# Kernel tuning notes

Hardware: AMD Instinct MI355X
Metric: run time of the kernel (lower is better)

## Reference

```python
import jax, jax.numpy as jnp
import numpy as np

# RosaAttention config constants
H = 16       # num_rosa_heads
KV = 4       # num_rosa_key_value_heads
QKB = 64     # num_rosa_query_key_bits
VB = 64      # num_rosa_value_bits
HID = 2048   # hidden_size
TAU = 1.0    # temperature buffer


def setup_inputs() -> dict:
    key = jax.random.key(0)
    ks = jax.random.split(key, 8)
    B, S = 2, 2048
    sc = 0.02
    return {
        "x": jax.random.normal(ks[0], (B, S, HID), jnp.float32),
        "attention_mask": jnp.ones((B, S), jnp.int32),
        "Wq": jax.random.normal(ks[1], (HID, H * QKB), jnp.float32) * sc,
        "Wk": jax.random.normal(ks[2], (HID, KV * QKB), jnp.float32) * sc,
        "Wv": jax.random.normal(ks[3], (HID, KV * VB), jnp.float32) * sc,
        "Wo": jax.random.normal(ks[4], (H * VB, HID), jnp.float32) * sc,
        "emb0": jnp.full((H, VB), -1e-05, jnp.float32),
        "emb1": jnp.full((H, VB), +1e-05, jnp.float32),
    }


def reference(x, attention_mask, Wq, Wk, Wv, Wo, emb0, emb1):
    B, S, _ = x.shape
    rep = H // KV
    # projections -> [b, s, heads, bits]
    xq = (x @ Wq).reshape(B, S, H, QKB)
    xk = (x @ Wk).reshape(B, S, KV, QKB)
    xv = (x @ Wv).reshape(B, S, KV, VB)
    # repeat_kv: each kv head repeated n_rep times contiguously
    xk = jnp.repeat(xk, rep, axis=2)   # [b, s, H, QKB]
    xv = jnp.repeat(xv, rep, axis=2)   # [b, s, H, VB]
    # soft bit quantization of q/k, tau-scaled bit-similarity score
    qb = jnp.tanh(xq)
    kb = jnp.tanh(xk)
    scores = jnp.einsum('bqhd,bkhd->bhqk', qb, kb) / (TAU * QKB)
    # causal mask + padding mask (mask True = attend)
    causal = jnp.tril(jnp.ones((S, S), bool))
    mask = causal[None, None] & attention_mask.astype(bool)[:, None, None, :]
    scores = jnp.where(mask, scores, jnp.finfo(scores.dtype).min)
    probs = jax.nn.softmax(scores, axis=-1)        # [b, h, q, k]
    # soft-binarized values: per-bit probabilities, attended, then mapped
    # through learned per-head bit embeddings emb0 (bit=0) / emb1 (bit=1)
    vp = jax.nn.sigmoid(xv)                        # [b, s, H, VB]
    ctx = jnp.einsum('bhqk,bkhv->bqhv', probs, vp) # [b, s, H, VB]
    out_bits = ctx * emb1[None, None] + (1.0 - ctx) * emb0[None, None]
    out = out_bits.reshape(B, S, H * VB) @ Wo      # [b, s, HID]
    return out
```

## Files before the change

### kernel.cpp

```cpp
#include <hip/hip_runtime.h>
#include <math.h>

typedef short bf16x8 __attribute__((ext_vector_type(8)));
typedef float f32x4 __attribute__((ext_vector_type(4)));
typedef unsigned int u32x2 __attribute__((ext_vector_type(2)));
typedef unsigned int u32x4 __attribute__((ext_vector_type(4)));

#define MFMA_BF16(A,B,C) __builtin_amdgcn_mfma_f32_16x16x32_bf16(A,B,C,0,0,0)

#define VMCNT(N) asm volatile("s_waitcnt vmcnt(" #N ")" ::: "memory")
#define RBAR() do { asm volatile("" ::: "memory"); __builtin_amdgcn_s_barrier(); \
                    asm volatile("" ::: "memory"); } while (0)


__device__ __forceinline__ unsigned short f2b(float x) {
    union { float f; unsigned int u; } v; v.f = x;
    unsigned int r = v.u + 0x7FFFu + ((v.u >> 16) & 1u);
    return (unsigned short)(r >> 16);
}

__device__ __forceinline__ unsigned int cvtpk(float lo, float hi) {
    unsigned int r;
    asm("v_cvt_pk_bf16_f32 %0, %1, %2" : "=v"(r) : "v"(lo), "v"(hi));
    return r;
}

__device__ __forceinline__ void gload16(const unsigned short* g, unsigned short* l) {
    __builtin_amdgcn_global_load_lds(
        (const __attribute__((address_space(1))) unsigned int*)(g),
        (__attribute__((address_space(3))) unsigned int*)(l),
        16, 0, 0);
}
__device__ __forceinline__ void gload4(const int* g, int* l) {
    __builtin_amdgcn_global_load_lds(
        (const __attribute__((address_space(1))) unsigned int*)(g),
        (__attribute__((address_space(3))) unsigned int*)(l),
        4, 0, 0);
}

__global__ __launch_bounds__(256) void conv_bf16(const float* __restrict__ s,
                                                 unsigned short* __restrict__ d, int n)
{
    int i = blockIdx.x * blockDim.x + threadIdx.x;
    int stride = gridDim.x * blockDim.x;
    for (int idx = i * 4; idx < n; idx += stride * 4) {
        float4 v = *(const float4*)(s + idx);
        ushort4 o;
        o.x = f2b(v.x); o.y = f2b(v.y); o.z = f2b(v.z); o.w = f2b(v.w);
        *(ushort4*)(d + idx) = o;
    }
}

__global__ __launch_bounds__(256) void transp_conv_qkv(const float* __restrict__ Wq,
                                                       const float* __restrict__ Wk,
                                                       const float* __restrict__ Wv,
                                                       unsigned short* __restrict__ dst)
{
    __shared__ float t[32][33];
    const int tx = threadIdx.x, ty = threadIdx.y;
    int bx = blockIdx.x;
    const float* src; int C, cb, dco;
    if (bx < 32)      { src = Wq; C = 1024; cb = bx;      dco = 0; }
    else if (bx < 40) { src = Wk; C = 256;  cb = bx - 32; dco = 1024; }
    else              { src = Wv; C = 256;  cb = bx - 40; dco = 1280; }
    const int c = cb * 32 + tx;
    const int r0 = blockIdx.y * 32;
#pragma unroll
    for (int i = 0; i < 4; ++i)
        t[ty + i * 8][tx] = src[(size_t)(r0 + ty + i * 8) * C + c];
    __syncthreads();
    const int cc = cb * 32 + ty;
#pragma unroll
    for (int i = 0; i < 4; ++i)
        dst[(size_t)(dco + cc + i * 8) * 2048 + r0 + tx] = f2b(t[tx][ty + i * 8]);
}

__global__ __launch_bounds__(256) void transp_conv(const float* __restrict__ src, int R, int C,
                                                   unsigned short* __restrict__ dst, int pitch)
{
    __shared__ float t[32][33];
    const int tx = threadIdx.x, ty = threadIdx.y;
    const int c = blockIdx.x * 32 + tx;
    const int r0 = blockIdx.y * 32;
#pragma unroll
    for (int i = 0; i < 4; ++i)
        t[ty + i * 8][tx] = src[(size_t)(r0 + ty + i * 8) * C + c];
    __syncthreads();
    const int cc = blockIdx.x * 32 + ty;
#pragma unroll
    for (int i = 0; i < 4; ++i)
        dst[(size_t)(cc + i * 8) * pitch + r0 + tx] = f2b(t[tx][ty + i * 8]);
}

__device__ __forceinline__ void stage_g(const unsigned short* AgL, const unsigned short* BgL,
                                        int K, int k0s,
                                        unsigned short* Asb, unsigned short* Bsb, int w)
{
#pragma unroll
    for (int t = 0; t < 4; ++t) {
        const int sub = t >> 1, half = t & 1;
        gload16(AgL + (size_t)(half * 16) * K + k0s + sub * 32,
                Asb + sub * 4096 + (w * 2 + half) * 512);
    }
#pragma unroll
    for (int kk = 0; kk < 2; ++kk)
        gload16(BgL + k0s + kk * 32, Bsb + kk * 2048 + w * 512);
}

template <int MODE>
__global__ __launch_bounds__(256, 3) void gemm_bt_mfma(
    const unsigned short* __restrict__ A,
    const unsigned short* __restrict__ Bt,
    int M, int N, int K,
    float* __restrict__ Cf,
    unsigned short* __restrict__ qh,
    unsigned short* __restrict__ kh,
    unsigned short* __restrict__ vtt)
{
    __shared__ __align__(16) unsigned short As[2][2 * 128 * 32];
    __shared__ __align__(16) unsigned short Bs[2][2 * 64 * 32];

    const int tid = threadIdx.x;
    const int w = tid >> 6, lane = tid & 63, l15 = lane & 15, quad = lane >> 4;
    const int wm = w & 1, wn = w >> 1;
    const int m0 = blockIdx.y * 128, n0 = blockIdx.x * 64;

    const int dsrow = lane >> 2;
    const int dscol = ((lane & 3) ^ ((lane >> 3) & 3)) * 8;
    const int sl8   = (((lane & 15) << 2) | ((lane >> 4) ^ ((lane >> 1) & 3))) * 8;

    f32x4 acc[4][2];
    const f32x4 zero4 = {0.f, 0.f, 0.f, 0.f};
#pragma unroll
    for (int i = 0; i < 4; ++i)
#pragma unroll
        for (int j = 0; j < 2; ++j) acc[i][j] = zero4;

    const unsigned short* AgL = A  + (size_t)(m0 + w * 32 + dsrow) * K + dscol;
    const unsigned short* BgL = Bt + (size_t)(n0 + w * 16 + dsrow) * K + dscol;

    const int NT = K >> 6;
    stage_g(AgL, BgL, K, 0, &As[0][0], &Bs[0][0], w);

    int cb = 0;
    for (int t = 0; t < NT; ++t) {
        if (t + 1 < NT) {
            stage_g(AgL, BgL, K, (t + 1) * 64, &As[cb ^ 1][0], &Bs[cb ^ 1][0], w);
            VMCNT(6);
        } else {
            VMCNT(0);
        }
        RBAR();

        bf16x8 af[4][2], bf[2][2];
#pragma unroll
        for (int kk = 0; kk < 2; ++kk) {
#pragma unroll
            for (int mt = 0; mt < 4; ++mt)
                af[mt][kk] = *(const bf16x8*)&As[cb][kk * 4096 + (wm * 4 + mt) * 512 + sl8];
#pragma unroll
            for (int nt = 0; nt < 2; ++nt)
                bf[nt][kk] = *(const bf16x8*)&Bs[cb][kk * 2048 + (wn * 2 + nt) * 512 + sl8];
        }
#pragma unroll
        for (int kk = 0; kk < 2; ++kk)
#pragma unroll
            for (int mt = 0; mt < 4; ++mt)
#pragma unroll
                for (int nt = 0; nt < 2; ++nt)
                    acc[mt][nt] = MFMA_BF16(af[mt][kk], bf[nt][kk], acc[mt][nt]);

        if (t + 1 < NT) RBAR();
        cb ^= 1;
    }

    if (MODE == 0) {
#pragma unroll
        for (int mt = 0; mt < 4; ++mt)
#pragma unroll
            for (int nt = 0; nt < 2; ++nt) {
                const int gn = n0 + wn * 32 + nt * 16 + l15;
#pragma unroll
                for (int r = 0; r < 4; ++r) {
                    const int gm = m0 + wm * 64 + mt * 16 + quad * 4 + r;
                    Cf[(size_t)gm * N + gn] = acc[mt][nt][r];
                }
            }
    } else {
        if (n0 < 1024) {
#pragma unroll
            for (int mt = 0; mt < 4; ++mt)
#pragma unroll
                for (int nt = 0; nt < 2; ++nt) {
                    const int gn = n0 + wn * 32 + nt * 16 + l15;
#pragma unroll
                    for (int r = 0; r < 4; ++r) {
                        const int gm = m0 + wm * 64 + mt * 16 + quad * 4 + r;
                        qh[(size_t)gm * 1024 + gn] = f2b(tanhf(acc[mt][nt][r]));
                    }
                }
        } else if (n0 < 1280) {
#pragma unroll
            for (int mt = 0; mt < 4; ++mt)
#pragma unroll
                for (int nt = 0; nt < 2; ++nt) {
                    const int gn = n0 + wn * 32 + nt * 16 + l15 - 1024;
#pragma unroll
                    for (int r = 0; r < 4; ++r) {
                        const int gm = m0 + wm * 64 + mt * 16 + quad * 4 + r;
                        kh[(size_t)gm * 256 + gn] = f2b(tanhf(acc[mt][nt][r]));
                    }
                }
        } else {
#pragma unroll
            for (int mt = 0; mt < 4; ++mt)
#pragma unroll
                for (int nt = 0; nt < 2; ++nt) {
                    const int gn = n0 + wn * 32 + nt * 16 + l15 - 1280;
                    const int g = gn >> 6, vv = gn & 63;
                    const int s0 = m0 + wm * 64 + mt * 16 + quad * 4;
                    const int b = s0 >> 11, sl = s0 & 2047;
                    ushort4 pk;
                    unsigned short* pp = (unsigned short*)&pk;
#pragma unroll
                    for (int r = 0; r < 4; ++r) {
                        float sv = 1.0f / (1.0f + __expf(-acc[mt][nt][r]));
                        pp[r] = f2b(sv);
                    }
                    *(ushort4*)&vtt[((size_t)(b * 4 + g) * 64 + vv) * 2048 + sl] = pk;
                }
        }
    }
}

__global__ __launch_bounds__(256, 3) void rosa_attn_mfma(
    const unsigned short* __restrict__ qh,
    const unsigned short* __restrict__ kh,
    const unsigned short* __restrict__ vtt,
    const int* __restrict__ amask,
    const float* __restrict__ emb0,
    const float* __restrict__ emb1,
    unsigned short* __restrict__ ob)
{
    __shared__ __align__(16) unsigned short Ks[2][2][2048];
    __shared__ __align__(16) unsigned short Vs[2][2][2048];
    __shared__ __align__(16) unsigned int   Ps[4][16][36];
    __shared__ int Mski[2][64];

    const int X = blockIdx.x;
    int qa, qb = 0, nq;
    if (X < 8)       { qa = 31 - X; nq = 1; }
    else if (X < 16) { qa = X + 8;  nq = 1; }
    else             { qa = X - 16; qb = 31 - X; nq = 2; }

    const int h = blockIdx.y, b = blockIdx.z, g = h >> 2;
    const int tid = threadIdx.x;
    const int w = tid >> 6, lane = tid & 63, l15 = lane & 15, quad = lane >> 4;

    const int dsrow = lane >> 2;
    const int dscol = ((lane & 3) ^ ((lane >> 3) & 3)) * 8;
    const int sl8   = (((lane & 15) << 2) | ((lane >> 4) ^ ((lane >> 1) & 3))) * 8;

    const unsigned short* kst = kh + (size_t)b * 2048 * 256 + g * 64
                               + (size_t)(w * 16 + dsrow) * 256 + dscol;
    const unsigned short* vst = vtt + ((size_t)(b * 4 + g) * 64 + w * 16 + dsrow) * 2048
                               + dscol;
    const int* mbase = amask + b * 2048;

    const f32x4 zero4 = {0.f, 0.f, 0.f, 0.f};
    const float cexp = 0.0225421100f;

#define STAGE_TILE(k0s, buf)                                               \
    {                                                                      \
        gload16(kst + (size_t)(k0s) * 256,      &Ks[buf][0][w * 512]);     \
        gload16(kst + (size_t)(k0s) * 256 + 32, &Ks[buf][1][w * 512]);     \
        gload16(vst + (k0s),                    &Vs[buf][0][w * 512]);     \
        gload16(vst + (k0s) + 32,               &Vs[buf][1][w * 512]);     \
        if (w == 0) gload4(mbase + (k0s) + lane, &Mski[buf][0]);           \
    }

    for (int hi = 0; hi < nq; ++hi) {
        const int qt = (hi == 0) ? qa : qb;
        const int q0 = qt * 64;
        const int nkt = qt + 1;
        const int qg = q0 + w * 16 + l15;

        const unsigned short* qrow = qh + ((size_t)(b * 2048 + qg) * 16 + h) * 64;
        const bf16x8 qf0 = *(const bf16x8*)(qrow + quad * 8);
        const bf16x8 qf1 = *(const bf16x8*)(qrow + 32 + quad * 8);

        f32x4 oacc[4];
#pragma unroll
        for (int t = 0; t < 4; ++t) oacc[t] = zero4;
        float psum = 0.0f;

        RBAR();
        STAGE_TILE(0, 0)

        int cb = 0;
        for (int kt = 0; kt < nkt; ++kt) {
            if (kt + 1 < nkt) {
                STAGE_TILE((kt + 1) * 64, cb ^ 1)
                if (w == 0) { VMCNT(5); } else { VMCNT(4); }
            } else {
                VMCNT(0);
            }
            RBAR();

            const bool diag = (kt == qt);
            const int ntlim = diag ? (w + 1) : 4;

#pragma unroll
            for (int nt = 0; nt < 4; ++nt) {
                u32x2 pk2;
                if (nt < ntlim) {
                    bf16x8 kf0 = *(const bf16x8*)&Ks[cb][0][nt * 512 + sl8];
                    bf16x8 kf1 = *(const bf16x8*)&Ks[cb][1][nt * 512 + sl8];
                    __builtin_amdgcn_s_setprio(1);
                    f32x4 sc = MFMA_BF16(kf0, qf0, zero4);
                    sc = MFMA_BF16(kf1, qf1, sc);
                    __builtin_amdgcn_s_setprio(0);
                    const int4 m4 = *(const int4*)&Mski[cb][nt * 16 + quad * 4];
                    const int* mm = (const int*)&m4;
                    const bool dnw = diag && (nt == w);
                    float p[4];
#pragma unroll
                    for (int r = 0; r < 4; ++r) {
                        float pv = __builtin_exp2f(sc[r] * cexp);
                        bool valid = (mm[r] != 0);
                        if (dnw) valid = valid && ((quad * 4 + r) <= l15);
                        pv = valid ? pv : 0.0f;
                        psum += pv;
                        p[r] = pv;
                    }
                    pk2[0] = cvtpk(p[0], p[1]);
                    pk2[1] = cvtpk(p[2], p[3]);
                } else {
                    pk2[0] = 0u; pk2[1] = 0u;
                }
                *(u32x2*)&Ps[w][l15][nt * 8 + quad * 2] = pk2;
            }

            const bf16x8 pf0 = __builtin_bit_cast(bf16x8, *(const u32x4*)&Ps[w][l15][quad * 4]);
            const bf16x8 pf1 = __builtin_bit_cast(bf16x8, *(const u32x4*)&Ps[w][l15][16 + quad * 4]);
            __builtin_amdgcn_s_setprio(1);
#pragma unroll
            for (int nt = 0; nt < 4; ++nt) {
                bf16x8 vf0 = *(const bf16x8*)&Vs[cb][0][nt * 512 + sl8];
                bf16x8 vf1 = *(const bf16x8*)&Vs[cb][1][nt * 512 + sl8];
                oacc[nt] = MFMA_BF16(pf0, vf0, oacc[nt]);
                oacc[nt] = MFMA_BF16(pf1, vf1, oacc[nt]);
            }
            __builtin_amdgcn_s_setprio(0);

            if (kt + 1 < nkt) {
                RBAR();
                cb ^= 1;
            }
        }

        float l = psum;
        l += __shfl_xor(l, 16);
        l += __shfl_xor(l, 32);
        float lq[4];
#pragma unroll
        for (int r = 0; r < 4; ++r) lq[r] = __shfl(l, quad * 4 + r);

#pragma unroll
        for (int nt = 0; nt < 4; ++nt) {
            const float e0 = emb0[h * 64 + nt * 16 + l15];
            const float e1 = emb1[h * 64 + nt * 16 + l15];
#pragma unroll
            for (int r = 0; r < 4; ++r) {
                const float ctx = oacc[nt][r] / lq[r];
                const float val = e0 + ctx * (e1 - e0);
                const size_t s_idx = (size_t)(b * 2048 + q0 + w * 16 + quad * 4 + r);
                ob[(s_idx * 16 + h) * 64 + nt * 16 + l15] = f2b(val);
            }
        }
    }
#undef STAGE_TILE
}

extern "C" void kernel_launch(void* const* d_in, const int* in_sizes, int n_in,
                              void* d_out, int out_size, void* d_ws, size_t ws_size,
                              hipStream_t stream)
{
    const float* x    = (const float*)d_in[0];
    const int*   amask= (const int*)d_in[1];
    const float* Wq   = (const float*)d_in[2];
    const float* Wk   = (const float*)d_in[3];
    const float* Wv   = (const float*)d_in[4];
    const float* Wo   = (const float*)d_in[5];
    const float* emb0 = (const float*)d_in[6];
    const float* emb1 = (const float*)d_in[7];
    float* out = (float*)d_out;

    char* base = (char*)d_ws;
    unsigned short* xh    = (unsigned short*)(base);
    unsigned short* ob    = xh;
    unsigned short* Wqkvt = (unsigned short*)(base + (16u << 20));
    unsigned short* Wot   = (unsigned short*)(base + (22u << 20));
    unsigned short* qh    = (unsigned short*)(base + (26u << 20));
    unsigned short* kh    = (unsigned short*)(base + (34u << 20));
    unsigned short* vtt   = (unsigned short*)(base + (36u << 20));

    conv_bf16<<<2048, 256, 0, stream>>>(x, xh, 4096 * 2048);
    transp_conv_qkv<<<dim3(48, 64), dim3(32, 8), 0, stream>>>(Wq, Wk, Wv, Wqkvt);
    transp_conv<<<dim3(64, 32), dim3(32, 8), 0, stream>>>(Wo, 1024, 2048, Wot, 1024);

    gemm_bt_mfma<1><<<dim3(24, 32), 256, 0, stream>>>(xh, Wqkvt, 4096, 1536, 2048,
                                                      nullptr, qh, kh, vtt);
    rosa_attn_mfma<<<dim3(24, 16, 2), 256, 0, stream>>>(qh, kh, vtt, amask, emb0, emb1, ob);
    gemm_bt_mfma<0><<<dim3(32, 32), 256, 0, stream>>>(ob, Wot, 4096, 2048, 1024,
                                                      out, nullptr, nullptr, nullptr);
}
```

Before: 235.3 us.

## Rework attention scheduling: one q-tile per block, precomputed mask flags, swizzled P

Each attention block now handles a single 64-row query tile, with tiles spread across blocks by a rotating pattern. This replaces the old pairing of a short and a long tile into one block, and the grid grows from 24 to 32 tiles per head. The padding mask is pre-scanned once per block into per-tile 'fully valid' flags, so full tiles skip the mask loads and selects, and the per-tile mask staging into LDS is removed. The P scratch buffer drops its padding in favour of an XOR swizzle, and the launch bounds ask for 4 blocks per CU. The risks are load imbalance from a plain causal distribution and register pressure under the higher occupancy target.

```diff
diff --git a/kernel.cpp b/kernel.cpp
--- a/kernel.cpp
+++ b/kernel.cpp
@@ -9,9 +9,9 @@
 #define MFMA_BF16(A,B,C) __builtin_amdgcn_mfma_f32_16x16x32_bf16(A,B,C,0,0,0)
 
 #define VMCNT(N) asm volatile("s_waitcnt vmcnt(" #N ")" ::: "memory")
+#define LGKM0()  asm volatile("s_waitcnt lgkmcnt(0)" ::: "memory")
 #define RBAR() do { asm volatile("" ::: "memory"); __builtin_amdgcn_s_barrier(); \
                     asm volatile("" ::: "memory"); } while (0)
-
 
 __device__ __forceinline__ unsigned short f2b(float x) {
     union { float f; unsigned int u; } v; v.f = x;
@@ -30,12 +30,6 @@
         (const __attribute__((address_space(1))) unsigned int*)(g),
         (__attribute__((address_space(3))) unsigned int*)(l),
         16, 0, 0);
-}
-__device__ __forceinline__ void gload4(const int* g, int* l) {
-    __builtin_amdgcn_global_load_lds(
-        (const __attribute__((address_space(1))) unsigned int*)(g),
-        (__attribute__((address_space(3))) unsigned int*)(l),
-        4, 0, 0);
 }
 
 __global__ __launch_bounds__(256) void conv_bf16(const float* __restrict__ s,
@@ -233,7 +227,7 @@
     }
 }
 
-__global__ __launch_bounds__(256, 3) void rosa_attn_mfma(
+__global__ __launch_bounds__(256, 4) void rosa_attn_mfma(
     const unsigned short* __restrict__ qh,
     const unsigned short* __restrict__ kh,
     const unsigned short* __restrict__ vtt,
@@ -244,22 +238,21 @@
 {
     __shared__ __align__(16) unsigned short Ks[2][2][2048];
     __shared__ __align__(16) unsigned short Vs[2][2][2048];
-    __shared__ __align__(16) unsigned int   Ps[4][16][36];
-    __shared__ int Mski[2][64];
-
-    const int X = blockIdx.x;
-    int qa, qb = 0, nq;
-    if (X < 8)       { qa = 31 - X; nq = 1; }
-    else if (X < 16) { qa = X + 8;  nq = 1; }
-    else             { qa = X - 16; qb = 31 - X; nq = 2; }
-
+    __shared__ __align__(16) unsigned int   Ps[4][16][32];
+
+    const int a = blockIdx.x & 7, m = blockIdx.x >> 3;
     const int h = blockIdx.y, b = blockIdx.z, g = h >> 2;
+    const int hb = h + 16 * b;
+    const int sel = (m + (hb >> 3)) & 3;
+    const int qt = (sel == 0) ? a : (sel == 1) ? 15 - a : (sel == 2) ? 16 + a : 31 - a;
+
     const int tid = threadIdx.x;
     const int w = tid >> 6, lane = tid & 63, l15 = lane & 15, quad = lane >> 4;
 
     const int dsrow = lane >> 2;
     const int dscol = ((lane & 3) ^ ((lane >> 3) & 3)) * 8;
     const int sl8   = (((lane & 15) << 2) | ((lane >> 4) ^ ((lane >> 1) & 3))) * 8;
+    const int pxor  = (l15 & 7) << 2;
 
     const unsigned short* kst = kh + (size_t)b * 2048 * 256 + g * 64
                                + (size_t)(w * 16 + dsrow) * 256 + dscol;
@@ -269,6 +262,20 @@
 
     const f32x4 zero4 = {0.f, 0.f, 0.f, 0.f};
     const float cexp = 0.0225421100f;
+
+    float cm[4];
+#pragma unroll
+    for (int r = 0; r < 4; ++r) cm[r] = (quad * 4 + r <= l15) ? 1.0f : 0.0f;
+
+    const int4 mv0 = *(const int4*)(mbase + tid * 8);
+    const int4 mv1 = *(const int4*)(mbase + tid * 8 + 4);
+
+    const int q0 = qt * 64;
+    const int nkt = qt + 1;
+
+    const unsigned short* qrow = qh + ((size_t)(b * 2048 + q0 + w * 16 + l15) * 16 + h) * 64;
+    const bf16x8 qf0 = *(const bf16x8*)(qrow + quad * 8);
+    const bf16x8 qf1 = *(const bf16x8*)(qrow + 32 + quad * 8);
 
 #define STAGE_TILE(k0s, buf)                                               \
     {                                                                      \
@@ -276,107 +283,117 @@
         gload16(kst + (size_t)(k0s) * 256 + 32, &Ks[buf][1][w * 512]);     \
         gload16(vst + (k0s),                    &Vs[buf][0][w * 512]);     \
         gload16(vst + (k0s) + 32,               &Vs[buf][1][w * 512]);     \
-        if (w == 0) gload4(mbase + (k0s) + lane, &Mski[buf][0]);           \
-    }
-
-    for (int hi = 0; hi < nq; ++hi) {
-        const int qt = (hi == 0) ? qa : qb;
-        const int q0 = qt * 64;
-        const int nkt = qt + 1;
-        const int qg = q0 + w * 16 + l15;
-
-        const unsigned short* qrow = qh + ((size_t)(b * 2048 + qg) * 16 + h) * 64;
-        const bf16x8 qf0 = *(const bf16x8*)(qrow + quad * 8);
-        const bf16x8 qf1 = *(const bf16x8*)(qrow + 32 + quad * 8);
-
-        f32x4 oacc[4];
-#pragma unroll
-        for (int t = 0; t < 4; ++t) oacc[t] = zero4;
-        float psum = 0.0f;
-
+    }
+
+    STAGE_TILE(0, 0)
+
+    const bool f8 = mv0.x && mv0.y && mv0.z && mv0.w && mv1.x && mv1.y && mv1.z && mv1.w;
+    const unsigned long long bal = __ballot(f8);
+    const bool bytefull = ((bal >> ((lane & 7) * 8)) & 0xFFull) == 0xFFull;
+    const unsigned long long bal2 = __ballot(bytefull && (lane < 8));
+    if (lane == 0) Ps[0][0][w] = (unsigned int)(bal2 & 0xFFull);
+    RBAR();
+    const unsigned int mflags = Ps[0][0][0] | (Ps[0][0][1] << 8)
+                              | (Ps[0][0][2] << 16) | (Ps[0][0][3] << 24);
+    LGKM0();
+    RBAR();
+
+    f32x4 oacc[4];
+#pragma unroll
+    for (int t = 0; t < 4; ++t) oacc[t] = zero4;
+    float psum = 0.0f;
+
+    int cb = 0;
+    for (int kt = 0; kt < nkt; ++kt) {
+        if (kt + 1 < nkt) {
+            STAGE_TILE((kt + 1) * 64, cb ^ 1)
+            VMCNT(4);
+        } else {
+            VMCNT(0);
+        }
         RBAR();
-        STAGE_TILE(0, 0)
-
-        int cb = 0;
-        for (int kt = 0; kt < nkt; ++kt) {
-            if (kt + 1 < nkt) {
-                STAGE_TILE((kt + 1) * 64, cb ^ 1)
-                if (w == 0) { VMCNT(5); } else { VMCNT(4); }
-            } else {
-                VMCNT(0);
-            }
-            RBAR();
-
-            const bool diag = (kt == qt);
-            const int ntlim = diag ? (w + 1) : 4;
-
-#pragma unroll
-            for (int nt = 0; nt < 4; ++nt) {
-                u32x2 pk2;
-                if (nt < ntlim) {
-                    bf16x8 kf0 = *(const bf16x8*)&Ks[cb][0][nt * 512 + sl8];
-                    bf16x8 kf1 = *(const bf16x8*)&Ks[cb][1][nt * 512 + sl8];
-                    __builtin_amdgcn_s_setprio(1);
-                    f32x4 sc = MFMA_BF16(kf0, qf0, zero4);
-                    sc = MFMA_BF16(kf1, qf1, sc);
-                    __builtin_amdgcn_s_setprio(0);
-                    const int4 m4 = *(const int4*)&Mski[cb][nt * 16 + quad * 4];
+
+        const int k0 = kt * 64;
+        const bool diag = (kt == qt);
+        const bool full = (mflags >> kt) & 1u;
+        const int ntlim = diag ? (w + 1) : 4;
+
+#pragma unroll
+        for (int nt = 0; nt < 4; ++nt) {
+            u32x2 pk2;
+            if (nt < ntlim) {
+                bf16x8 kf0 = *(const bf16x8*)&Ks[cb][0][nt * 512 + sl8];
+                bf16x8 kf1 = *(const bf16x8*)&Ks[cb][1][nt * 512 + sl8];
+                __builtin_amdgcn_s_setprio(1);
+                f32x4 sc = MFMA_BF16(kf0, qf0, zero4);
+                sc = MFMA_BF16(kf1, qf1, sc);
+                __builtin_amdgcn_s_setprio(0);
+                const bool dnw = diag && (nt == w);
+                float p[4];
+                if (full) {
+                    if (dnw) {
+#pragma unroll
+                        for (int r = 0; r < 4; ++r)
+                            p[r] = __builtin_exp2f(sc[r] * cexp) * cm[r];
+                    } else {
+#pragma unroll
+                        for (int r = 0; r < 4; ++r)
+                            p[r] = __builtin_exp2f(sc[r] * cexp);
+                    }
+                } else {
+                    const int4 m4 = *(const int4*)(mbase + k0 + nt * 16 + quad * 4);
                     const int* mm = (const int*)&m4;
-                    const bool dnw = diag && (nt == w);
-                    float p[4];
 #pragma unroll
                     for (int r = 0; r < 4; ++r) {
                         float pv = __builtin_exp2f(sc[r] * cexp);
-                        bool valid = (mm[r] != 0);
-                        if (dnw) valid = valid && ((quad * 4 + r) <= l15);
-                        pv = valid ? pv : 0.0f;
-                        psum += pv;
-                        p[r] = pv;
+                        if (dnw) pv *= cm[r];
+                        p[r] = (mm[r] != 0) ? pv : 0.0f;
                     }
-                    pk2[0] = cvtpk(p[0], p[1]);
-                    pk2[1] = cvtpk(p[2], p[3]);
-                } else {
-                    pk2[0] = 0u; pk2[1] = 0u;
                 }
-                *(u32x2*)&Ps[w][l15][nt * 8 + quad * 2] = pk2;
+                psum += (p[0] + p[1]) + (p[2] + p[3]);
+                pk2[0] = cvtpk(p[0], p[1]);
+                pk2[1] = cvtpk(p[2], p[3]);
+            } else {
+                pk2[0] = 0u; pk2[1] = 0u;
             }
-
-            const bf16x8 pf0 = __builtin_bit_cast(bf16x8, *(const u32x4*)&Ps[w][l15][quad * 4]);
-            const bf16x8 pf1 = __builtin_bit_cast(bf16x8, *(const u32x4*)&Ps[w][l15][16 + quad * 4]);
-            __builtin_amdgcn_s_setprio(1);
-#pragma unroll
-            for (int nt = 0; nt < 4; ++nt) {
-                bf16x8 vf0 = *(const bf16x8*)&Vs[cb][0][nt * 512 + sl8];
-                bf16x8 vf1 = *(const bf16x8*)&Vs[cb][1][nt * 512 + sl8];
-                oacc[nt] = MFMA_BF16(pf0, vf0, oacc[nt]);
-                oacc[nt] = MFMA_BF16(pf1, vf1, oacc[nt]);
-            }
-            __builtin_amdgcn_s_setprio(0);
-
-            if (kt + 1 < nkt) {
-                RBAR();
-                cb ^= 1;
-            }
-        }
-
-        float l = psum;
-        l += __shfl_xor(l, 16);
-        l += __shfl_xor(l, 32);
-        float lq[4];
-#pragma unroll
-        for (int r = 0; r < 4; ++r) lq[r] = __shfl(l, quad * 4 + r);
-
+            *(u32x2*)&Ps[w][l15][(nt * 8 + quad * 2) ^ pxor] = pk2;
+        }
+
+        const bf16x8 pf0 = __builtin_bit_cast(bf16x8, *(const u32x4*)&Ps[w][l15][(quad * 4) ^ pxor]);
+        const bf16x8 pf1 = __builtin_bit_cast(bf16x8, *(const u32x4*)&Ps[w][l15][(16 + quad * 4) ^ pxor]);
+        __builtin_amdgcn_s_setprio(1);
 #pragma unroll
         for (int nt = 0; nt < 4; ++nt) {
-            const float e0 = emb0[h * 64 + nt * 16 + l15];
-            const float e1 = emb1[h * 64 + nt * 16 + l15];
-#pragma unroll
-            for (int r = 0; r < 4; ++r) {
-                const float ctx = oacc[nt][r] / lq[r];
-                const float val = e0 + ctx * (e1 - e0);
-                const size_t s_idx = (size_t)(b * 2048 + q0 + w * 16 + quad * 4 + r);
-                ob[(s_idx * 16 + h) * 64 + nt * 16 + l15] = f2b(val);
-            }
+            bf16x8 vf0 = *(const bf16x8*)&Vs[cb][0][nt * 512 + sl8];
+            bf16x8 vf1 = *(const bf16x8*)&Vs[cb][1][nt * 512 + sl8];
+            oacc[nt] = MFMA_BF16(pf0, vf0, oacc[nt]);
+            oacc[nt] = MFMA_BF16(pf1, vf1, oacc[nt]);
+        }
+        __builtin_amdgcn_s_setprio(0);
+
+        if (kt + 1 < nkt) {
+            RBAR();
+            cb ^= 1;
+        }
+    }
+
+    float l = psum;
+    l += __shfl_xor(l, 16);
+    l += __shfl_xor(l, 32);
+    float lq[4];
+#pragma unroll
+    for (int r = 0; r < 4; ++r) lq[r] = __shfl(l, quad * 4 + r);
+
+#pragma unroll
+    for (int nt = 0; nt < 4; ++nt) {
+        const float e0 = emb0[h * 64 + nt * 16 + l15];
+        const float e1 = emb1[h * 64 + nt * 16 + l15];
+#pragma unroll
+        for (int r = 0; r < 4; ++r) {
+            const float ctx = oacc[nt][r] / lq[r];
+            const float val = e0 + ctx * (e1 - e0);
+            const size_t s_idx = (size_t)(b * 2048 + q0 + w * 16 + quad * 4 + r);
+            ob[(s_idx * 16 + h) * 64 + nt * 16 + l15] = f2b(val);
         }
     }
 #undef STAGE_TILE
@@ -411,7 +428,7 @@
 
     gemm_bt_mfma<1><<<dim3(24, 32), 256, 0, stream>>>(xh, Wqkvt, 4096, 1536, 2048,
                                                       nullptr, qh, kh, vtt);
-    rosa_attn_mfma<<<dim3(24, 16, 2), 256, 0, stream>>>(qh, kh, vtt, amask, emb0, emb1, ob);
+    rosa_attn_mfma<<<dim3(32, 16, 2), 256, 0, stream>>>(qh, kh, vtt, amask, emb0, emb1, ob);
     gemm_bt_mfma<0><<<dim3(32, 32), 256, 0, stream>>>(ob, Wot, 4096, 2048, 1024,
                                                       out, nullptr, nullptr, nullptr);
 }
```

Measured after the change: 229.8 us. 1.02x faster.
